# Performance work log

Measured on AMD Instinct MI355X. Metric: run time of the kernel, lower is better.

Reference implementation:

```python
import jax, jax.numpy as jnp
import numpy as np
from jax import lax

VOCAB = 50000   # marker token id == vocab_size
EMB = 1024
HID = 1024      # bidirectional total
HD = HID // 2   # per-direction hidden
LAYERS = 2
B, T = 32, 512


def setup_inputs() -> dict:
    key = jax.random.key(0)
    ks = jax.random.split(key, 12)
    seq = jax.random.randint(ks[0], (B, T), 1, VOCAB)
    pos = jax.random.randint(ks[1], (B,), 0, T)
    seq = seq.at[jnp.arange(B), pos].set(VOCAB)  # exactly one marker per row
    label = (jax.random.uniform(ks[2], (B,)) > 0.5).astype(jnp.float32)
    s = 1.0 / np.sqrt(HD)
    w_emb = jax.random.normal(ks[3], (VOCAB + 1, EMB), jnp.float32) * 0.05
    w_ih = jax.random.uniform(ks[4], (LAYERS, 2, 4 * HD, EMB), jnp.float32, -s, s)
    w_hh = jax.random.uniform(ks[5], (LAYERS, 2, 4 * HD, HD), jnp.float32, -s, s)
    b = jax.random.uniform(ks[6], (LAYERS, 2, 4 * HD), jnp.float32, -s, s)
    w1 = jax.random.normal(ks[7], (HD, HID), jnp.float32) * 0.03
    b1 = jnp.zeros((HD,), jnp.float32)
    w2 = jax.random.normal(ks[8], (1, HD), jnp.float32) * 0.03
    b2 = jnp.zeros((1,), jnp.float32)
    return {"seq": seq, "label": label, "w_emb": w_emb, "w_ih": w_ih,
            "w_hh": w_hh, "b": b, "w1": w1, "b1": b1, "w2": w2, "b2": b2}


def _run_dir(x, Wih, Whh, bb, reverse):
    # x: [B,T,In]; precompute input contribution to all 4 gates (i,f,g,o order, torch layout)
    gx = jnp.einsum('bti,gi->btg', x, Wih) + bb  # [B,T,4*HD]

    def step(carry, g):
        h, c = carry
        g = g + h @ Whh.T
        i, f, gg, o = jnp.split(g, 4, axis=-1)
        c = jax.nn.sigmoid(f) * c + jax.nn.sigmoid(i) * jnp.tanh(gg)
        h = jax.nn.sigmoid(o) * jnp.tanh(c)
        return (h, c), h

    h0 = jnp.zeros((x.shape[0], HD), x.dtype)
    _, hs = lax.scan(step, (h0, h0), gx.transpose(1, 0, 2), reverse=reverse)
    return hs.transpose(1, 0, 2)  # [B,T,HD], time order preserved


def reference(seq, label, w_emb, w_ih, w_hh, b, w1, b1, w2, b2):
    emb = w_emb.at[0].set(0.0)[seq]  # padding_idx=0 -> zero vector
    x = emb
    for l in range(LAYERS):
        fwd = _run_dir(x, w_ih[l, 0], w_hh[l, 0], b[l, 0], False)
        bwd = _run_dir(x, w_ih[l, 1], w_hh[l, 1], b[l, 1], True)
        x = jnp.concatenate([fwd, bwd], axis=-1)  # [B,T,HID]
    # masked_select at the single marker position per row -> [B,HID]
    idx = jnp.argmax(seq == VOCAB, axis=1)
    hidden = x[jnp.arange(x.shape[0]), idx]
    h = jnp.tanh(hidden @ w1.T + b1)
    logit = (h @ w2.T + b2)[:, 0]
    # BCEWithLogits, mean reduction: softplus(z) - z*y
    return jnp.mean(jax.nn.softplus(logit) - logit * label)
```

## Files before the change

kernel.cpp:

```cpp
#include <hip/hip_runtime.h>
#include <stdint.h>

typedef unsigned short u16;
typedef __bf16 bf16x8 __attribute__((ext_vector_type(8)));
typedef float  f32x4  __attribute__((ext_vector_type(4)));

#define GPTR(p) ((const __attribute__((address_space(1))) void*)(p))
#define LPTR(p) ((__attribute__((address_space(3))) void*)(p))

__device__ __forceinline__ u16 f2bf(float f) {
  uint32_t u = __float_as_uint(f);
  u += 0x7FFFu + ((u >> 16) & 1u);
  return (u16)(u >> 16);
}
__device__ __forceinline__ float bf2f(u16 h) {
  return __uint_as_float(((uint32_t)h) << 16);
}
__device__ __forceinline__ float sigf(float x) { return 1.0f / (1.0f + __expf(-x)); }
__device__ __forceinline__ float tanhf_(float x) { return 1.0f - 2.0f / (__expf(2.0f * x) + 1.0f); }

__global__ void k_emb(const int* __restrict__ seq, const float* __restrict__ wemb,
                      u16* __restrict__ x1) {
  const int row = blockIdx.x;
  const int tok = seq[row];
  float4 v = ((const float4*)(wemb + (size_t)tok * 1024))[threadIdx.x];
  uint32_t lo = (uint32_t)f2bf(v.x) | ((uint32_t)f2bf(v.y) << 16);
  uint32_t hi = (uint32_t)f2bf(v.z) | ((uint32_t)f2bf(v.w) << 16);
  *(uint2*)(x1 + (size_t)row * 1024 + threadIdx.x * 4) = make_uint2(lo, hi);
}

__global__ void k_idx(const int* __restrict__ seq, int* __restrict__ idxb) {
  const int tid = threadIdx.x;
  const int b = tid >> 3, part = tid & 7;
  for (int t = part * 64; t < part * 64 + 64; ++t)
    if (seq[b * 512 + t] == 50000) idxb[b] = t;
}

__global__ void k_cast(const float* __restrict__ src, u16* __restrict__ dst) {
  const int i = blockIdx.x * 256 + threadIdx.x;
  float4 v = ((const float4*)src)[i];
  uint32_t lo = (uint32_t)f2bf(v.x) | ((uint32_t)f2bf(v.y) << 16);
  uint32_t hi = (uint32_t)f2bf(v.z) | ((uint32_t)f2bf(v.w) << 16);
  *(uint2*)(dst + (size_t)i * 4) = make_uint2(lo, hi);
}

__global__ __launch_bounds__(256) void k_gemm(
    const u16* __restrict__ X, const u16* __restrict__ W,
    const float* __restrict__ bias, u16* __restrict__ gx)
{
  __shared__ u16 As[128][32];
  __shared__ u16 Bs[128][32];
  const int tid = threadIdx.x;
  const int lane = tid & 63;
  const int wv = tid >> 6;
  const int wm = wv >> 1, wn = wv & 1;
  const int bm = blockIdx.x, bn = blockIdx.y;
  const int srow = tid >> 2;
  const int scg = (tid & 3) * 8;
  const u16* Xb = X + (size_t)bm * 128 * 1024;
  const u16* Wb = W + (size_t)bn * 128 * 1024;
  f32x4 acc[4][4] = {};
  for (int k0 = 0; k0 < 1024; k0 += 32) {
    __builtin_amdgcn_global_load_lds(GPTR(Xb + (size_t)srow * 1024 + k0 + scg),        LPTR(&As[srow][scg]),       16, 0, 0);
    __builtin_amdgcn_global_load_lds(GPTR(Xb + (size_t)(srow + 64) * 1024 + k0 + scg), LPTR(&As[srow + 64][scg]), 16, 0, 0);
    __builtin_amdgcn_global_load_lds(GPTR(Wb + (size_t)srow * 1024 + k0 + scg),        LPTR(&Bs[srow][scg]),       16, 0, 0);
    __builtin_amdgcn_global_load_lds(GPTR(Wb + (size_t)(srow + 64) * 1024 + k0 + scg), LPTR(&Bs[srow + 64][scg]), 16, 0, 0);
    __syncthreads();
    const int kg = (lane >> 4) * 8;
    bf16x8 a4[4], b4[4];
    #pragma unroll
    for (int mt = 0; mt < 4; ++mt) a4[mt] = *(const bf16x8*)&As[wm * 64 + mt * 16 + (lane & 15)][kg];
    #pragma unroll
    for (int nt = 0; nt < 4; ++nt) b4[nt] = *(const bf16x8*)&Bs[wn * 64 + nt * 16 + (lane & 15)][kg];
    #pragma unroll
    for (int mt = 0; mt < 4; ++mt)
      #pragma unroll
      for (int nt = 0; nt < 4; ++nt)
        acc[mt][nt] = __builtin_amdgcn_mfma_f32_16x16x32_bf16(a4[mt], b4[nt], acc[mt][nt], 0, 0, 0);
    __syncthreads();
  }
  #pragma unroll
  for (int mt = 0; mt < 4; ++mt) {
    const int mbase = bm * 128 + wm * 64 + mt * 16 + ((lane >> 4) << 2);
    #pragma unroll
    for (int nt = 0; nt < 4; ++nt) {
      const int n = bn * 128 + wn * 64 + nt * 16 + (lane & 15);
      const float bi = bias[n];
      const int d = n >> 11;
      const int nn = n & 2047;
      const int q = nn >> 9;
      const int j = nn & 511;
      const int col = (j >> 4) * 64 + q * 16 + (j & 15);
      #pragma unroll
      for (int r = 0; r < 4; ++r) {
        const int mm = mbase + r;
        const int b = mm >> 9, t = mm & 511;
        gx[((size_t)(d * 512 + t) * 32 + b) * 2048 + col] = f2bf(acc[mt][nt][r] + bi);
      }
    }
  }
}

__global__ __launch_bounds__(256, 1) void k_rec(
    const u16* __restrict__ gx, const float* __restrict__ whh,
    u16* __restrict__ xout, u16* hstep)
{
  const int bid = blockIdx.x;
  const int dir = bid >> 5;
  const int db = bid & 31;
  const int j0 = db * 16;
  const int tid = threadIdx.x;
  const int lane = tid & 63;
  const int wv = tid >> 6;
  const int mh = wv >> 1, nh = wv & 1;
  const int R = lane & 15;
  const int ks = lane >> 4;

  __shared__ float G[2][32][68];

  bf16x8 bw[2][16];
  {
    #pragma unroll
    for (int nt = 0; nt < 2; ++nt) {
      const int q = nh * 2 + nt;
      const float* wp = whh + ((size_t)dir * 2048 + q * 512 + j0 + R) * 512 + ks * 8;
      #pragma unroll
      for (int kt = 0; kt < 16; ++kt) {
        float4 v0 = *(const float4*)(wp + kt * 32);
        float4 v1 = *(const float4*)(wp + kt * 32 + 4);
        union { u16 u[8]; bf16x8 v; } t;
        t.u[0] = f2bf(v0.x); t.u[1] = f2bf(v0.y); t.u[2] = f2bf(v0.z); t.u[3] = f2bf(v0.w);
        t.u[4] = f2bf(v1.x); t.u[5] = f2bf(v1.y); t.u[6] = f2bf(v1.z); t.u[7] = f2bf(v1.w);
        bw[nt][kt] = t.v;
      }
    }
  }

  const int eb = tid >> 3;
  const int pr = (tid & 7) * 2;
  float c0 = 0.f, c1 = 0.f;

  const size_t dirbase = (size_t)dir * 512 * 16384;
  const u16* apbase = hstep + dirbase + (size_t)(ks >> 1) * 512 + (mh * 16 + R) * 16 + (ks & 1) * 8;
  const u16* gxeb   = gx + ((size_t)dir * 512 * 32 + eb) * 2048 + db * 64 + pr;

  uint32_t gq[4];
  {
    const int t0 = dir ? 511 : 0;
    const uint32_t* g0 = (const uint32_t*)(gxeb + (size_t)t0 * 65536);
    gq[0] = g0[0]; gq[1] = g0[8]; gq[2] = g0[16]; gq[3] = g0[24];
  }

  for (int s = 0; s < 512; ++s) {
    const int tcur = dir ? (511 - s) : s;
    const int gb = s & 1;
    f32x4 acc0 = {0.f,0.f,0.f,0.f}, acc1 = {0.f,0.f,0.f,0.f};

    if (s) {
      const size_t slot = (size_t)(s - 1) * 16384;
      const u16* ap = apbase + slot;
      uint4 afu[16];
      #pragma unroll
      for (int kt = 0; kt < 16; ++kt)
        asm volatile("global_load_dwordx4 %0, %1, off sc0 sc1"
                     : "=v"(afu[kt]) : "v"(ap + kt * 1024) : "memory");
      asm volatile("s_waitcnt vmcnt(0)" ::: "memory");
      __builtin_amdgcn_sched_barrier(0);
      while (true) {
        unsigned mask = 0;
        #pragma unroll
        for (int kt = 0; kt < 16; ++kt) {
          int ok = (afu[kt].x != 0xFFFFFFFFu) && (afu[kt].y != 0xFFFFFFFFu) &&
                   (afu[kt].z != 0xFFFFFFFFu) && (afu[kt].w != 0xFFFFFFFFu);
          if (!__all(ok)) mask |= 1u << kt;
        }
        if (!mask) break;
        #pragma unroll
        for (int kt = 0; kt < 16; ++kt)
          if (mask & (1u << kt))
            asm volatile("global_load_dwordx4 %0, %1, off sc0 sc1"
                         : "=v"(afu[kt]) : "v"(ap + kt * 1024) : "memory");
        asm volatile("s_waitcnt vmcnt(0)" ::: "memory");
        __builtin_amdgcn_sched_barrier(0);
      }
      f32x4 a0 = {0.f,0.f,0.f,0.f}, a1 = {0.f,0.f,0.f,0.f};
      f32x4 b0 = {0.f,0.f,0.f,0.f}, b1 = {0.f,0.f,0.f,0.f};
      #pragma unroll
      for (int kt = 0; kt < 16; kt += 2) {
        bf16x8 x = __builtin_bit_cast(bf16x8, afu[kt]);
        bf16x8 y = __builtin_bit_cast(bf16x8, afu[kt + 1]);
        a0 = __builtin_amdgcn_mfma_f32_16x16x32_bf16(x, bw[0][kt],     a0, 0, 0, 0);
        a1 = __builtin_amdgcn_mfma_f32_16x16x32_bf16(x, bw[1][kt],     a1, 0, 0, 0);
        b0 = __builtin_amdgcn_mfma_f32_16x16x32_bf16(y, bw[0][kt + 1], b0, 0, 0, 0);
        b1 = __builtin_amdgcn_mfma_f32_16x16x32_bf16(y, bw[1][kt + 1], b1, 0, 0, 0);
      }
      acc0 = a0 + b0;
      acc1 = a1 + b1;
    }

    #pragma unroll
    for (int r = 0; r < 4; ++r) {
      G[gb][mh * 16 + (lane >> 4) * 4 + r][nh * 32 + (lane & 15)]      = acc0[r];
      G[gb][mh * 16 + (lane >> 4) * 4 + r][nh * 32 + 16 + (lane & 15)] = acc1[r];
    }
    __syncthreads();

    {
      float i0 = G[gb][eb][pr]      + bf2f((u16)(gq[0] & 0xFFFF));
      float i1 = G[gb][eb][pr + 1]  + bf2f((u16)(gq[0] >> 16));
      float f0 = G[gb][eb][pr + 16] + bf2f((u16)(gq[1] & 0xFFFF));
      float f1 = G[gb][eb][pr + 17] + bf2f((u16)(gq[1] >> 16));
      float g0 = G[gb][eb][pr + 32] + bf2f((u16)(gq[2] & 0xFFFF));
      float g1 = G[gb][eb][pr + 33] + bf2f((u16)(gq[2] >> 16));
      float o0 = G[gb][eb][pr + 48] + bf2f((u16)(gq[3] & 0xFFFF));
      float o1 = G[gb][eb][pr + 49] + bf2f((u16)(gq[3] >> 16));
      c0 = sigf(f0) * c0 + sigf(i0) * tanhf_(g0);
      c1 = sigf(f1) * c1 + sigf(i1) * tanhf_(g1);
      float h0 = sigf(o0) * tanhf_(c0);
      float h1 = sigf(o1) * tanhf_(c1);
      uint32_t hp = (uint32_t)f2bf(h0) | ((uint32_t)f2bf(h1) << 16);
      u16* hdst = hstep + dirbase + (size_t)s * 16384 + (size_t)db * 512 + eb * 16 + pr;
      asm volatile("global_store_dword %0, %1, off sc0 sc1"
                   :: "v"(hdst), "v"(hp) : "memory");
      *(uint32_t*)(xout + ((size_t)eb * 512 + tcur) * 1024 + dir * 512 + j0 + pr) = hp;
    }
    if (s < 511) {
      const int tn = dir ? (511 - (s + 1)) : (s + 1);
      const uint32_t* gn = (const uint32_t*)(gxeb + (size_t)tn * 65536);
      gq[0] = gn[0]; gq[1] = gn[8]; gq[2] = gn[16]; gq[3] = gn[24];
    }
  }
}

__global__ void k_cls1(const u16* __restrict__ x3, const int* __restrict__ idxb,
                       const float* __restrict__ w1, const float* __restrict__ b1,
                       float* __restrict__ h1) {
  __shared__ u16 hid[32][1024];
  const int tid = threadIdx.x;
  for (int g = tid; g < 4096; g += 256) {
    const int b = g >> 7;
    const int c8 = (g & 127) * 8;
    *(uint4*)&hid[b][c8] = *(const uint4*)(x3 + ((size_t)b * 512 + idxb[b]) * 1024 + c8);
  }
  __syncthreads();
  for (int p = tid; p < 1024; p += 256) {
    const int j = blockIdx.x * 32 + (p >> 5);
    const int b = p & 31;
    const float4* wr = (const float4*)(w1 + (size_t)j * 1024);
    float s = 0.f;
    for (int k4 = 0; k4 < 256; ++k4) {
      float4 wv = wr[k4];
      const int k = k4 * 4;
      s += bf2f(hid[b][k]) * wv.x + bf2f(hid[b][k + 1]) * wv.y
         + bf2f(hid[b][k + 2]) * wv.z + bf2f(hid[b][k + 3]) * wv.w;
    }
    h1[b * 512 + j] = tanhf_(s + b1[j]);
  }
}

__global__ void k_cls2(const float* __restrict__ h1, const float* __restrict__ w2,
                       const float* __restrict__ b2, const float* __restrict__ label,
                       float* __restrict__ out) {
  const int lane = threadIdx.x;
  float loss = 0.f;
  for (int b = 0; b < 32; ++b) {
    float s = 0.f;
    for (int k = lane; k < 512; k += 64) s += h1[b * 512 + k] * w2[k];
    for (int off = 32; off; off >>= 1) s += __shfl_down(s, off);
    if (lane == 0) {
      const float z = s + b2[0];
      const float y = label[b];
      const float sp = fmaxf(z, 0.f) + log1pf(__expf(-fabsf(z)));
      loss += sp - z * y;
    }
  }
  if (lane == 0) out[0] = loss / 32.0f;
}

extern "C" void kernel_launch(void* const* d_in, const int* in_sizes, int n_in,
                              void* d_out, int out_size, void* d_ws, size_t ws_size,
                              hipStream_t stream) {
  const int*   seq   = (const int*)  d_in[0];
  const float* label = (const float*)d_in[1];
  const float* wemb  = (const float*)d_in[2];
  const float* wih   = (const float*)d_in[3];
  const float* whh   = (const float*)d_in[4];
  const float* bb    = (const float*)d_in[5];
  const float* w1    = (const float*)d_in[6];
  const float* b1    = (const float*)d_in[7];
  const float* w2    = (const float*)d_in[8];
  const float* b2    = (const float*)d_in[9];

  u16* x1   = (u16*)d_ws;
  u16* x2   = x1 + (size_t)16777216;
  u16* gxb  = x2 + (size_t)16777216;
  u16* wb   = gxb + (size_t)67108864;
  float* h1 = (float*)(wb + 4194304);
  int* idxb = (int*)(h1 + 16384);

  k_emb<<<16384, 256, 0, stream>>>(seq, wemb, x1);
  k_idx<<<1, 256, 0, stream>>>(seq, idxb);
  k_cast<<<4096, 256, 0, stream>>>(wih, wb);
  k_gemm<<<dim3(128, 32), 256, 0, stream>>>(x1, wb, bb, gxb);
  hipMemsetAsync(x1, 0xFF, (size_t)33554432, stream);
  k_rec<<<64, 256, 0, stream>>>(gxb, whh, x2, x1);
  k_cast<<<4096, 256, 0, stream>>>(wih + 4194304, wb);
  k_gemm<<<dim3(128, 32), 256, 0, stream>>>(x2, wb, bb + 4096, gxb);
  hipMemsetAsync(x2, 0xFF, (size_t)33554432, stream);
  k_rec<<<64, 256, 0, stream>>>(gxb, whh + 2097152, x1, x2);
  k_cls1<<<16, 256, 0, stream>>>(x1, idxb, w1, b1, h1);
  k_cls2<<<1, 64, 0, stream>>>(h1, w2, b2, label, (float*)d_out);
}
```

Baseline: 4.677 ms.

## Restructure LSTM recurrence to per-wave full gates and drop the xout write

The recurrent kernel now runs with 2 waves, and each wave computes all four gates for its 16 batch rows directly in MFMA registers. This removes the shared-memory gate exchange and the block barrier on every step. The gate precompute layout is permuted so each lane fetches its i/f/g/o values as contiguous pairs. The separate time-major output write is dropped, and the next layer's GEMM and the classifier read the step-indexed h buffer directly through a remapped address. Readiness polling now checks a single probe word first and only falls back to per-tile rechecks, which cuts spin cost but depends on store ordering across the tile.

```diff
diff --git a/kernel.cpp b/kernel.cpp
--- a/kernel.cpp
+++ b/kernel.cpp
@@ -44,6 +44,7 @@
   *(uint2*)(dst + (size_t)i * 4) = make_uint2(lo, hi);
 }
 
+template<int REMAP>
 __global__ __launch_bounds__(256) void k_gemm(
     const u16* __restrict__ X, const u16* __restrict__ W,
     const float* __restrict__ bias, u16* __restrict__ gx)
@@ -57,12 +58,26 @@
   const int bm = blockIdx.x, bn = blockIdx.y;
   const int srow = tid >> 2;
   const int scg = (tid & 3) * 8;
-  const u16* Xb = X + (size_t)bm * 128 * 1024;
   const u16* Wb = W + (size_t)bn * 128 * 1024;
   f32x4 acc[4][4] = {};
   for (int k0 = 0; k0 < 1024; k0 += 32) {
-    __builtin_amdgcn_global_load_lds(GPTR(Xb + (size_t)srow * 1024 + k0 + scg),        LPTR(&As[srow][scg]),       16, 0, 0);
-    __builtin_amdgcn_global_load_lds(GPTR(Xb + (size_t)(srow + 64) * 1024 + k0 + scg), LPTR(&As[srow + 64][scg]), 16, 0, 0);
+    if constexpr (REMAP == 0) {
+      const u16* Xb = X + (size_t)bm * 128 * 1024;
+      __builtin_amdgcn_global_load_lds(GPTR(Xb + (size_t)srow * 1024 + k0 + scg),        LPTR(&As[srow][scg]),       16, 0, 0);
+      __builtin_amdgcn_global_load_lds(GPTR(Xb + (size_t)(srow + 64) * 1024 + k0 + scg), LPTR(&As[srow + 64][scg]), 16, 0, 0);
+    } else {
+      const int b = bm >> 2;
+      const int dirk = k0 >> 9;
+      const int jj = (k0 & 511) + scg;
+      const int t1 = (bm & 3) * 128 + srow;
+      const int t2 = t1 + 64;
+      const int s1 = dirk ? 511 - t1 : t1;
+      const int s2 = dirk ? 511 - t2 : t2;
+      const u16* src1 = X + (size_t)dirk * 8388608 + (size_t)s1 * 16384 + (jj >> 4) * 512 + b * 16 + (jj & 15);
+      const u16* src2 = X + (size_t)dirk * 8388608 + (size_t)s2 * 16384 + (jj >> 4) * 512 + b * 16 + (jj & 15);
+      __builtin_amdgcn_global_load_lds(GPTR(src1), LPTR(&As[srow][scg]),       16, 0, 0);
+      __builtin_amdgcn_global_load_lds(GPTR(src2), LPTR(&As[srow + 64][scg]), 16, 0, 0);
+    }
     __builtin_amdgcn_global_load_lds(GPTR(Wb + (size_t)srow * 1024 + k0 + scg),        LPTR(&Bs[srow][scg]),       16, 0, 0);
     __builtin_amdgcn_global_load_lds(GPTR(Wb + (size_t)(srow + 64) * 1024 + k0 + scg), LPTR(&Bs[srow + 64][scg]), 16, 0, 0);
     __syncthreads();
@@ -90,20 +105,19 @@
       const int nn = n & 2047;
       const int q = nn >> 9;
       const int j = nn & 511;
-      const int col = (j >> 4) * 64 + q * 16 + (j & 15);
+      const int db2 = j >> 4, col = j & 15;
       #pragma unroll
       for (int r = 0; r < 4; ++r) {
         const int mm = mbase + r;
         const int b = mm >> 9, t = mm & 511;
-        gx[((size_t)(d * 512 + t) * 32 + b) * 2048 + col] = f2bf(acc[mt][nt][r] + bi);
+        gx[(((size_t)(d * 512 + t) * 32 + db2) * 16 + col) * 128 + b * 4 + q] = f2bf(acc[mt][nt][r] + bi);
       }
     }
   }
 }
 
-__global__ __launch_bounds__(256, 1) void k_rec(
-    const u16* __restrict__ gx, const float* __restrict__ whh,
-    u16* __restrict__ xout, u16* hstep)
+__global__ __launch_bounds__(128, 1) void k_rec(
+    const u16* __restrict__ gx, const float* __restrict__ whh, u16* hstep)
 {
   const int bid = blockIdx.x;
   const int dir = bid >> 5;
@@ -111,136 +125,142 @@
   const int j0 = db * 16;
   const int tid = threadIdx.x;
   const int lane = tid & 63;
-  const int wv = tid >> 6;
-  const int mh = wv >> 1, nh = wv & 1;
+  const int w = tid >> 6;
   const int R = lane & 15;
   const int ks = lane >> 4;
 
-  __shared__ float G[2][32][68];
-
-  bf16x8 bw[2][16];
-  {
-    #pragma unroll
-    for (int nt = 0; nt < 2; ++nt) {
-      const int q = nh * 2 + nt;
-      const float* wp = whh + ((size_t)dir * 2048 + q * 512 + j0 + R) * 512 + ks * 8;
-      #pragma unroll
-      for (int kt = 0; kt < 16; ++kt) {
-        float4 v0 = *(const float4*)(wp + kt * 32);
-        float4 v1 = *(const float4*)(wp + kt * 32 + 4);
-        union { u16 u[8]; bf16x8 v; } t;
-        t.u[0] = f2bf(v0.x); t.u[1] = f2bf(v0.y); t.u[2] = f2bf(v0.z); t.u[3] = f2bf(v0.w);
-        t.u[4] = f2bf(v1.x); t.u[5] = f2bf(v1.y); t.u[6] = f2bf(v1.z); t.u[7] = f2bf(v1.w);
-        bw[nt][kt] = t.v;
-      }
-    }
-  }
-
-  const int eb = tid >> 3;
-  const int pr = (tid & 7) * 2;
-  float c0 = 0.f, c1 = 0.f;
-
-  const size_t dirbase = (size_t)dir * 512 * 16384;
-  const u16* apbase = hstep + dirbase + (size_t)(ks >> 1) * 512 + (mh * 16 + R) * 16 + (ks & 1) * 8;
-  const u16* gxeb   = gx + ((size_t)dir * 512 * 32 + eb) * 2048 + db * 64 + pr;
-
-  uint32_t gq[4];
+  bf16x8 bw[4][16];
+  #pragma unroll
+  for (int q = 0; q < 4; ++q) {
+    const float* wp = whh + ((size_t)dir * 2048 + q * 512 + j0 + R) * 512 + ks * 8;
+    #pragma unroll
+    for (int kt = 0; kt < 16; ++kt) {
+      float4 v0 = *(const float4*)(wp + kt * 32);
+      float4 v1 = *(const float4*)(wp + kt * 32 + 4);
+      union { u16 u[8]; bf16x8 v; } t;
+      t.u[0] = f2bf(v0.x); t.u[1] = f2bf(v0.y); t.u[2] = f2bf(v0.z); t.u[3] = f2bf(v0.w);
+      t.u[4] = f2bf(v1.x); t.u[5] = f2bf(v1.y); t.u[6] = f2bf(v1.z); t.u[7] = f2bf(v1.w);
+      bw[q][kt] = t.v;
+    }
+  }
+
+  const int rbase = w * 16 + ks * 4;
+  float c0 = 0.f, c1 = 0.f, c2 = 0.f, c3 = 0.f;
+  const size_t dirbase = (size_t)dir * 8388608;
+  const u16* apbase = hstep + dirbase + (size_t)(ks >> 1) * 512 + (w * 16 + R) * 16 + (ks & 1) * 8;
+  const u16* prbase = hstep + dirbase + (size_t)(lane & 31) * 512 + (w * 16 + 15) * 16 + 14;
+  const u16* gxbase = gx + (((size_t)dir * 16384 + (size_t)db) * 16 + R) * 128 + rbase * 4;
+
+  uint2 gq0, gq1, gq2, gq3;
   {
     const int t0 = dir ? 511 : 0;
-    const uint32_t* g0 = (const uint32_t*)(gxeb + (size_t)t0 * 65536);
-    gq[0] = g0[0]; gq[1] = g0[8]; gq[2] = g0[16]; gq[3] = g0[24];
+    const u16* g = gxbase + (size_t)t0 * 65536;
+    gq0 = *(const uint2*)(g);     gq1 = *(const uint2*)(g + 4);
+    gq2 = *(const uint2*)(g + 8); gq3 = *(const uint2*)(g + 12);
   }
 
   for (int s = 0; s < 512; ++s) {
-    const int tcur = dir ? (511 - s) : s;
-    const int gb = s & 1;
-    f32x4 acc0 = {0.f,0.f,0.f,0.f}, acc1 = {0.f,0.f,0.f,0.f};
+    f32x4 acci = {0.f,0.f,0.f,0.f}, accf = {0.f,0.f,0.f,0.f};
+    f32x4 accg = {0.f,0.f,0.f,0.f}, acco = {0.f,0.f,0.f,0.f};
 
     if (s) {
       const size_t slot = (size_t)(s - 1) * 16384;
       const u16* ap = apbase + slot;
+      const u16* pp = prbase + slot;
+      uint32_t fv;
+      asm volatile("global_load_dword %0, %1, off sc0 sc1\n\ts_waitcnt vmcnt(0)"
+                   : "=v"(fv) : "v"(pp) : "memory");
+      const int pass1 = __all((int)(((fv & 0xFFFFu) != 0xFFFFu) & ((fv >> 16) != 0xFFFFu)));
       uint4 afu[16];
       #pragma unroll
       for (int kt = 0; kt < 16; ++kt)
         asm volatile("global_load_dwordx4 %0, %1, off sc0 sc1"
                      : "=v"(afu[kt]) : "v"(ap + kt * 1024) : "memory");
-      asm volatile("s_waitcnt vmcnt(0)" ::: "memory");
+      if (!pass1) {
+        while (true) {
+          asm volatile("global_load_dword %0, %1, off sc0 sc1\n\ts_waitcnt vmcnt(0)"
+                       : "=v"(fv) : "v"(pp) : "memory");
+          if (__all((int)(((fv & 0xFFFFu) != 0xFFFFu) & ((fv >> 16) != 0xFFFFu)))) break;
+        }
+      } else {
+        asm volatile("s_waitcnt vmcnt(0)" ::: "memory");
+      }
       __builtin_amdgcn_sched_barrier(0);
-      while (true) {
-        unsigned mask = 0;
-        #pragma unroll
-        for (int kt = 0; kt < 16; ++kt) {
-          int ok = (afu[kt].x != 0xFFFFFFFFu) && (afu[kt].y != 0xFFFFFFFFu) &&
-                   (afu[kt].z != 0xFFFFFFFFu) && (afu[kt].w != 0xFFFFFFFFu);
-          if (!__all(ok)) mask |= 1u << kt;
+      if (!pass1) {
+        while (true) {
+          unsigned mask = 0;
+          #pragma unroll
+          for (int kt = 0; kt < 16; ++kt) {
+            const uint4 xx = afu[kt];
+            int ok = (int)(((xx.x & 0xFFFFu) != 0xFFFFu) & ((xx.x >> 16) != 0xFFFFu)
+                         & ((xx.y & 0xFFFFu) != 0xFFFFu) & ((xx.y >> 16) != 0xFFFFu)
+                         & ((xx.z & 0xFFFFu) != 0xFFFFu) & ((xx.z >> 16) != 0xFFFFu)
+                         & ((xx.w & 0xFFFFu) != 0xFFFFu) & ((xx.w >> 16) != 0xFFFFu));
+            if (!__all(ok)) mask |= 1u << kt;
+          }
+          if (!mask) break;
+          #pragma unroll
+          for (int kt = 0; kt < 16; ++kt)
+            if (mask & (1u << kt))
+              asm volatile("global_load_dwordx4 %0, %1, off sc0 sc1"
+                           : "=v"(afu[kt]) : "v"(ap + kt * 1024) : "memory");
+          asm volatile("s_waitcnt vmcnt(0)" ::: "memory");
+          __builtin_amdgcn_sched_barrier(0);
         }
-        if (!mask) break;
-        #pragma unroll
-        for (int kt = 0; kt < 16; ++kt)
-          if (mask & (1u << kt))
-            asm volatile("global_load_dwordx4 %0, %1, off sc0 sc1"
-                         : "=v"(afu[kt]) : "v"(ap + kt * 1024) : "memory");
-        asm volatile("s_waitcnt vmcnt(0)" ::: "memory");
-        __builtin_amdgcn_sched_barrier(0);
       }
-      f32x4 a0 = {0.f,0.f,0.f,0.f}, a1 = {0.f,0.f,0.f,0.f};
-      f32x4 b0 = {0.f,0.f,0.f,0.f}, b1 = {0.f,0.f,0.f,0.f};
       #pragma unroll
-      for (int kt = 0; kt < 16; kt += 2) {
-        bf16x8 x = __builtin_bit_cast(bf16x8, afu[kt]);
-        bf16x8 y = __builtin_bit_cast(bf16x8, afu[kt + 1]);
-        a0 = __builtin_amdgcn_mfma_f32_16x16x32_bf16(x, bw[0][kt],     a0, 0, 0, 0);
-        a1 = __builtin_amdgcn_mfma_f32_16x16x32_bf16(x, bw[1][kt],     a1, 0, 0, 0);
-        b0 = __builtin_amdgcn_mfma_f32_16x16x32_bf16(y, bw[0][kt + 1], b0, 0, 0, 0);
-        b1 = __builtin_amdgcn_mfma_f32_16x16x32_bf16(y, bw[1][kt + 1], b1, 0, 0, 0);
+      for (int kt = 0; kt < 16; ++kt) {
+        bf16x8 a = __builtin_bit_cast(bf16x8, afu[kt]);
+        acci = __builtin_amdgcn_mfma_f32_16x16x32_bf16(a, bw[0][kt], acci, 0, 0, 0);
+        accf = __builtin_amdgcn_mfma_f32_16x16x32_bf16(a, bw[1][kt], accf, 0, 0, 0);
+        accg = __builtin_amdgcn_mfma_f32_16x16x32_bf16(a, bw[2][kt], accg, 0, 0, 0);
+        acco = __builtin_amdgcn_mfma_f32_16x16x32_bf16(a, bw[3][kt], acco, 0, 0, 0);
       }
-      acc0 = a0 + b0;
-      acc1 = a1 + b1;
-    }
-
-    #pragma unroll
-    for (int r = 0; r < 4; ++r) {
-      G[gb][mh * 16 + (lane >> 4) * 4 + r][nh * 32 + (lane & 15)]      = acc0[r];
-      G[gb][mh * 16 + (lane >> 4) * 4 + r][nh * 32 + 16 + (lane & 15)] = acc1[r];
-    }
-    __syncthreads();
-
-    {
-      float i0 = G[gb][eb][pr]      + bf2f((u16)(gq[0] & 0xFFFF));
-      float i1 = G[gb][eb][pr + 1]  + bf2f((u16)(gq[0] >> 16));
-      float f0 = G[gb][eb][pr + 16] + bf2f((u16)(gq[1] & 0xFFFF));
-      float f1 = G[gb][eb][pr + 17] + bf2f((u16)(gq[1] >> 16));
-      float g0 = G[gb][eb][pr + 32] + bf2f((u16)(gq[2] & 0xFFFF));
-      float g1 = G[gb][eb][pr + 33] + bf2f((u16)(gq[2] >> 16));
-      float o0 = G[gb][eb][pr + 48] + bf2f((u16)(gq[3] & 0xFFFF));
-      float o1 = G[gb][eb][pr + 49] + bf2f((u16)(gq[3] >> 16));
-      c0 = sigf(f0) * c0 + sigf(i0) * tanhf_(g0);
-      c1 = sigf(f1) * c1 + sigf(i1) * tanhf_(g1);
-      float h0 = sigf(o0) * tanhf_(c0);
-      float h1 = sigf(o1) * tanhf_(c1);
-      uint32_t hp = (uint32_t)f2bf(h0) | ((uint32_t)f2bf(h1) << 16);
-      u16* hdst = hstep + dirbase + (size_t)s * 16384 + (size_t)db * 512 + eb * 16 + pr;
-      asm volatile("global_store_dword %0, %1, off sc0 sc1"
-                   :: "v"(hdst), "v"(hp) : "memory");
-      *(uint32_t*)(xout + ((size_t)eb * 512 + tcur) * 1024 + dir * 512 + j0 + pr) = hp;
-    }
+    }
+
+    u16* hb = hstep + dirbase + (size_t)s * 16384 + db * 512 + rbase * 16 + R;
+#define CELL(RR, CC, GQ)                                                        \
+    {                                                                           \
+      float i = acci[RR] + bf2f((u16)(GQ.x & 0xFFFF));                          \
+      float f = accf[RR] + bf2f((u16)(GQ.x >> 16));                             \
+      float g = accg[RR] + bf2f((u16)(GQ.y & 0xFFFF));                          \
+      float o = acco[RR] + bf2f((u16)(GQ.y >> 16));                             \
+      CC = sigf(f) * CC + sigf(i) * tanhf_(g);                                  \
+      uint32_t hv = (uint32_t)f2bf(sigf(o) * tanhf_(CC));                       \
+      asm volatile("global_store_short %0, %1, off sc0 sc1"                     \
+                   :: "v"(hb + RR * 16), "v"(hv) : "memory");                   \
+    }
+    CELL(0, c0, gq0)
+    CELL(1, c1, gq1)
+    CELL(2, c2, gq2)
+    CELL(3, c3, gq3)
+#undef CELL
+
     if (s < 511) {
       const int tn = dir ? (511 - (s + 1)) : (s + 1);
-      const uint32_t* gn = (const uint32_t*)(gxeb + (size_t)tn * 65536);
-      gq[0] = gn[0]; gq[1] = gn[8]; gq[2] = gn[16]; gq[3] = gn[24];
-    }
-  }
-}
-
-__global__ void k_cls1(const u16* __restrict__ x3, const int* __restrict__ idxb,
+      const u16* g = gxbase + (size_t)tn * 65536;
+      gq0 = *(const uint2*)(g);     gq1 = *(const uint2*)(g + 4);
+      gq2 = *(const uint2*)(g + 8); gq3 = *(const uint2*)(g + 12);
+    }
+  }
+}
+
+__global__ void k_cls1(const u16* __restrict__ hs, const int* __restrict__ idxb,
                        const float* __restrict__ w1, const float* __restrict__ b1,
                        float* __restrict__ h1) {
   __shared__ u16 hid[32][1024];
   const int tid = threadIdx.x;
-  for (int g = tid; g < 4096; g += 256) {
-    const int b = g >> 7;
-    const int c8 = (g & 127) * 8;
-    *(uint4*)&hid[b][c8] = *(const uint4*)(x3 + ((size_t)b * 512 + idxb[b]) * 1024 + c8);
+  for (int g = tid; g < 2048; g += 256) {
+    const int b = g >> 6;
+    const int jc = g & 63;
+    const int dir = jc >> 5;
+    const int j16 = jc & 31;
+    const int t = idxb[b];
+    const int s = dir ? 511 - t : t;
+    const u16* src = hs + (size_t)dir * 8388608 + (size_t)s * 16384 + j16 * 512 + b * 16;
+    u16* dst = &hid[b][dir * 512 + j16 * 16];
+    *(uint4*)(dst)     = *(const uint4*)(src);
+    *(uint4*)(dst + 8) = *(const uint4*)(src + 8);
   }
   __syncthreads();
   for (int p = tid; p < 1024; p += 256) {
@@ -301,13 +321,13 @@
   k_emb<<<16384, 256, 0, stream>>>(seq, wemb, x1);
   k_idx<<<1, 256, 0, stream>>>(seq, idxb);
   k_cast<<<4096, 256, 0, stream>>>(wih, wb);
-  k_gemm<<<dim3(128, 32), 256, 0, stream>>>(x1, wb, bb, gxb);
+  k_gemm<0><<<dim3(128, 32), 256, 0, stream>>>(x1, wb, bb, gxb);
+  hipMemsetAsync(x2, 0xFF, (size_t)33554432, stream);
+  k_rec<<<64, 128, 0, stream>>>(gxb, whh, x2);
+  k_cast<<<4096, 256, 0, stream>>>(wih + 4194304, wb);
+  k_gemm<1><<<dim3(128, 32), 256, 0, stream>>>(x2, wb, bb + 4096, gxb);
   hipMemsetAsync(x1, 0xFF, (size_t)33554432, stream);
-  k_rec<<<64, 256, 0, stream>>>(gxb, whh, x2, x1);
-  k_cast<<<4096, 256, 0, stream>>>(wih + 4194304, wb);
-  k_gemm<<<dim3(128, 32), 256, 0, stream>>>(x2, wb, bb + 4096, gxb);
-  hipMemsetAsync(x2, 0xFF, (size_t)33554432, stream);
-  k_rec<<<64, 256, 0, stream>>>(gxb, whh + 2097152, x1, x2);
+  k_rec<<<64, 128, 0, stream>>>(gxb, whh + 2097152, x1);
   k_cls1<<<16, 256, 0, stream>>>(x1, idxb, w1, b1, h1);
   k_cls2<<<1, 64, 0, stream>>>(h1, w2, b2, label, (float*)d_out);
 }
```

After: 7.291 ms. 55.9% more time.
